# Performance work log

Hardware: AMD Instinct MI355X
Metric: run time of the kernel (lower is better)

The kernel has to match this reference:

```python
import jax, jax.numpy as jnp
import numpy as np

D = 1024
H = 16
DH = D // H
LN_EPS = 1e-5


def setup_inputs() -> dict:
    key = jax.random.key(0)
    ks = jax.random.split(key, 8)
    B, L = 32768, 3
    q = jax.random.normal(ks[0], (B, 1, D), dtype=jnp.float32)
    x = jax.random.normal(ks[1], (B, L, D), dtype=jnp.float32)
    s = 0.02  # weight init scale
    Wq = jax.random.normal(ks[2], (D, D), dtype=jnp.float32) * s
    Wk = jax.random.normal(ks[3], (D, D), dtype=jnp.float32) * s
    Wv = jax.random.normal(ks[4], (D, D), dtype=jnp.float32) * s
    Wr = jax.random.normal(ks[5], (D, D), dtype=jnp.float32) * s
    Wo = jax.random.normal(ks[6], (D, D), dtype=jnp.float32) * s
    ln_gamma = jnp.ones((D,), dtype=jnp.float32)
    ln_beta = jnp.zeros((D,), dtype=jnp.float32)
    return {"q": q, "x": x, "Wq": Wq, "Wk": Wk, "Wv": Wv, "Wr": Wr,
            "Wo": Wo, "ln_gamma": ln_gamma, "ln_beta": ln_beta}


def _layer_norm(y, gamma, beta):
    mu = jnp.mean(y, axis=-1, keepdims=True)
    var = jnp.mean(jnp.square(y - mu), axis=-1, keepdims=True)
    return (y - mu) * jax.lax.rsqrt(var + LN_EPS) * gamma + beta


def reference(q, x, Wq, Wk, Wv, Wr, Wo, ln_gamma, ln_beta):
    # torch Linear(no bias): y = inp @ W^T
    Q = jnp.einsum('bqd,ed->bqe', q, Wq)            # [B,1,D]
    K = jnp.einsum('bld,ed->ble', x, Wk)            # [B,L,D]
    V = jnp.einsum('bld,ed->ble', x, Wv)
    R = jnp.einsum('bld,ed->ble', x, Wr)
    V_eff = jax.nn.sigmoid(R) * V                   # gated V
    B, L = x.shape[0], x.shape[1]
    Qh = Q.reshape(B, 1, H, DH).transpose(0, 2, 1, 3)   # [B,H,1,Dh]
    Kh = K.reshape(B, L, H, DH).transpose(0, 2, 1, 3)   # [B,H,L,Dh]
    Vh = V_eff.reshape(B, L, H, DH).transpose(0, 2, 1, 3)
    scores = jnp.einsum('bhqd,bhld->bhql', Qh, Kh) / jnp.sqrt(jnp.float32(DH))
    attn = jax.nn.softmax(scores, axis=-1)              # [B,H,1,L]; dropout=eval no-op
    out = jnp.einsum('bhql,bhld->bhqd', attn, Vh)       # [B,H,1,Dh]
    out = out.transpose(0, 2, 1, 3).reshape(B, 1, D)
    out = jnp.einsum('bqd,ed->bqe', out, Wo)
    out = _layer_norm(q + out, ln_gamma, ln_beta)
    return out, attn
```

## Files before the change

kernel.cpp:

```cpp
#include <hip/hip_runtime.h>
#include <math.h>


using half8   = __attribute__((ext_vector_type(8))) _Float16;
using half4   = __attribute__((ext_vector_type(4))) _Float16;
using floatx4 = __attribute__((ext_vector_type(4))) float;

#define BTOT 32768
#define DM   1024
#define NH   16
#define LSEQ 3

__device__ __forceinline__ void gload_lds16(const void* g, void* l) {
  __builtin_amdgcn_global_load_lds(
      (const __attribute__((address_space(1))) void*)g,
      (__attribute__((address_space(3))) void*)l, 16, 0, 0);
}

__global__ __launch_bounds__(256) void acvt(
    const float* __restrict__ xc, _Float16* __restrict__ x16,
    const float* __restrict__ qc, _Float16* __restrict__ q16, int xblocks)
{
  const int blk = blockIdx.x;
  const float* src;
  _Float16* dst;
  size_t o;
  if (blk < xblocks) {
    o = ((size_t)blk * 256 + threadIdx.x) * 4;
    src = xc; dst = x16;
  } else {
    o = ((size_t)(blk - xblocks) * 256 + threadIdx.x) * 4;
    src = qc; dst = q16;
  }
  floatx4 a = *(const floatx4*)(src + o);
  half4 h;
  h[0] = (_Float16)a[0]; h[1] = (_Float16)a[1];
  h[2] = (_Float16)a[2]; h[3] = (_Float16)a[3];
  *(half4*)(dst + o) = h;
}

__global__ __launch_bounds__(256) void wconv(
    const float* __restrict__ Wq, const float* __restrict__ Wk,
    const float* __restrict__ Wv, const float* __restrict__ Wr,
    const float* __restrict__ Wo,
    _Float16* __restrict__ Wq16, _Float16* __restrict__ Wkvr16,
    _Float16* __restrict__ Wo16)
{
  const int i = blockIdx.x * 256 + threadIdx.x;
  const size_t o = (size_t)i * 4;
  const size_t M1 = (size_t)1024 * 1024;
  floatx4 a;
  half4 h;
#define CVT(SRC, DST, OFF)                                        \
  a = *(const floatx4*)((SRC) + o);                               \
  h[0] = (_Float16)a[0]; h[1] = (_Float16)a[1];                   \
  h[2] = (_Float16)a[2]; h[3] = (_Float16)a[3];                   \
  *(half4*)((DST) + (OFF) + o) = h;
  CVT(Wq, Wq16, 0)
  CVT(Wo, Wo16, 0)
  CVT(Wk, Wkvr16, 0)
  CVT(Wv, Wkvr16, M1)
  CVT(Wr, Wkvr16, 2 * M1)
#undef CVT
}

template <bool OUT_HALF>
__global__ __launch_bounds__(256) void gemm_bt(
    const _Float16* __restrict__ A, const _Float16* __restrict__ Bw,
    void* __restrict__ Cout, int M, int N, int K)
{
  __shared__ __attribute__((aligned(16))) char As[128 * 128];
  __shared__ __attribute__((aligned(16))) char Bs[128 * 128];

  const int tid  = threadIdx.x;
  const int lane = tid & 63;
  const int wave = tid >> 6;
  const int wr = wave >> 1, wc = wave & 1;
  const int l15 = lane & 15, lk = lane >> 4;

  const int nwg = gridDim.x * gridDim.y;
  int wgid = blockIdx.y * gridDim.x + blockIdx.x;
  wgid = (wgid & 7) * (nwg >> 3) + (wgid >> 3);
  const int bx = wgid % gridDim.x;
  const int by = wgid / gridDim.x;

  const int col0 = bx * 128;
  const int row0 = by * 128;

  floatx4 acc[4][4] = {};

  const int nK = K >> 6;
  for (int kt = 0; kt < nK; ++kt) {
    const int k0 = kt << 6;
    {
      const char* gA = (const char*)A + ((size_t)row0 * K + k0) * 2;
      const char* gB = (const char*)Bw + ((size_t)col0 * K + k0) * 2;
      #pragma unroll
      for (int it = 0; it < 4; ++it) {
        const int off = it * 4096 + tid * 16;
        const int row = off >> 7;
        const int ch  = (off >> 4) & 7;
        const int sch = ch ^ (row & 7);
        gload_lds16(gA + (size_t)row * ((size_t)K * 2) + (sch << 4), As + off);
        gload_lds16(gB + (size_t)row * ((size_t)K * 2) + (sch << 4), Bs + off);
      }
    }
    __syncthreads();
    #pragma unroll
    for (int kk = 0; kk < 64; kk += 32) {
      half8 af[4], bf[4];
      const int c = (kk >> 3) + lk;
      #pragma unroll
      for (int m = 0; m < 4; ++m) {
        const int rw = wr * 64 + m * 16 + l15;
        af[m] = *(const half8*)(As + rw * 128 + ((c ^ (rw & 7)) << 4));
      }
      #pragma unroll
      for (int n = 0; n < 4; ++n) {
        const int rw = wc * 64 + n * 16 + l15;
        bf[n] = *(const half8*)(Bs + rw * 128 + ((c ^ (rw & 7)) << 4));
      }
      #pragma unroll
      for (int m = 0; m < 4; ++m)
        #pragma unroll
        for (int n = 0; n < 4; ++n)
          acc[m][n] = __builtin_amdgcn_mfma_f32_16x16x32_f16(
              af[m], bf[n], acc[m][n], 0, 0, 0);
    }
    __syncthreads();
  }
  #pragma unroll
  for (int m = 0; m < 4; ++m) {
    const int rbase = row0 + wr * 64 + m * 16 + (lk << 2);
    #pragma unroll
    for (int r = 0; r < 4; ++r) {
      const size_t rowoff = (size_t)(rbase + r) * N;
      #pragma unroll
      for (int n = 0; n < 4; ++n) {
        const int col = col0 + wc * 64 + n * 16 + l15;
        const float v = acc[m][n][r];
        if constexpr (OUT_HALF)
          ((_Float16*)Cout)[rowoff + col] = (_Float16)v;
        else
          ((float*)Cout)[rowoff + col] = v;
      }
    }
  }
}

__global__ __launch_bounds__(256) void attn_kernel(
    const _Float16* __restrict__ Q16, const _Float16* __restrict__ KVR,
    _Float16* __restrict__ AV16, float* __restrict__ attn_out,
    size_t batch0)
{
  const int lane = threadIdx.x & 63;
  const int wave = threadIdx.x >> 6;
  const size_t b = (size_t)blockIdx.x * 4 + wave;
  const int h = lane >> 2, p = lane & 3;
  const int doff = h * 64 + p * 16;

  float qv[16];
  {
    const half8* qp = (const half8*)(Q16 + b * 1024 + doff);
    half8 q0 = qp[0], q1 = qp[1];
    #pragma unroll
    for (int i = 0; i < 8; ++i) { qv[i] = (float)q0[i]; qv[8 + i] = (float)q1[i]; }
  }
  float sc[LSEQ];
  #pragma unroll
  for (int l = 0; l < LSEQ; ++l) {
    const half8* kp = (const half8*)(KVR + (b * 3 + l) * 3072 + doff);
    half8 k0 = kp[0], k1 = kp[1];
    float d = 0.f;
    #pragma unroll
    for (int i = 0; i < 8; ++i)
      d += qv[i] * (float)k0[i] + qv[8 + i] * (float)k1[i];
    d += __shfl_xor(d, 1);
    d += __shfl_xor(d, 2);
    sc[l] = d * 0.125f;
  }
  const float mx = fmaxf(sc[0], fmaxf(sc[1], sc[2]));
  const float e0 = __expf(sc[0] - mx), e1 = __expf(sc[1] - mx),
              e2 = __expf(sc[2] - mx);
  const float inv = 1.f / (e0 + e1 + e2);
  const float at0 = e0 * inv, at1 = e1 * inv, at2 = e2 * inv;
  if (p == 0) {
    float* ao = attn_out + ((batch0 + b) * NH + h) * LSEQ;
    ao[0] = at0; ao[1] = at1; ao[2] = at2;
  }
  const float atw[LSEQ] = {at0, at1, at2};
  float av[16] = {};
  #pragma unroll
  for (int l = 0; l < LSEQ; ++l) {
    const half8* vp = (const half8*)(KVR + (b * 3 + l) * 3072 + 1024 + doff);
    const half8* rp = (const half8*)(KVR + (b * 3 + l) * 3072 + 2048 + doff);
    half8 v0 = vp[0], v1 = vp[1], r0 = rp[0], r1 = rp[1];
    #pragma unroll
    for (int i = 0; i < 8; ++i) {
      const float g0 = 1.f / (1.f + __expf(-(float)r0[i]));
      const float g1 = 1.f / (1.f + __expf(-(float)r1[i]));
      av[i]     += atw[l] * g0 * (float)v0[i];
      av[8 + i] += atw[l] * g1 * (float)v1[i];
    }
  }
  half8 o0, o1;
  #pragma unroll
  for (int i = 0; i < 8; ++i) { o0[i] = (_Float16)av[i]; o1[i] = (_Float16)av[8 + i]; }
  half8* op = (half8*)(AV16 + b * 1024 + doff);
  op[0] = o0; op[1] = o1;
}

__global__ __launch_bounds__(256) void ln_kernel(
    const float* __restrict__ qres, const float* __restrict__ outlin,
    const float* __restrict__ gamma, const float* __restrict__ beta,
    float* __restrict__ out)
{
  const int lane = threadIdx.x & 63;
  const size_t r = (size_t)blockIdx.x * 4 + (threadIdx.x >> 6);
  const size_t base = r * 1024 + lane * 16;
  floatx4 y[4];
  float s = 0.f, ss = 0.f;
  #pragma unroll
  for (int i = 0; i < 4; ++i) {
    floatx4 a  = *(const floatx4*)(qres + base + i * 4);
    floatx4 bb = *(const floatx4*)(outlin + base + i * 4);
    y[i] = a + bb;
    #pragma unroll
    for (int j = 0; j < 4; ++j) { s += y[i][j]; ss += y[i][j] * y[i][j]; }
  }
  #pragma unroll
  for (int o = 1; o < 64; o <<= 1) {
    s  += __shfl_xor(s, o);
    ss += __shfl_xor(ss, o);
  }
  const float mu  = s * (1.f / 1024.f);
  const float var = ss * (1.f / 1024.f) - mu * mu;
  const float rs  = rsqrtf(var + 1e-5f);
  #pragma unroll
  for (int i = 0; i < 4; ++i) {
    floatx4 g  = *(const floatx4*)(gamma + lane * 16 + i * 4);
    floatx4 be = *(const floatx4*)(beta + lane * 16 + i * 4);
    floatx4 o;
    #pragma unroll
    for (int j = 0; j < 4; ++j)
      o[j] = (y[i][j] - mu) * rs * g[j] + be[j];
    *(floatx4*)(out + base + i * 4) = o;
  }
}

extern "C" void kernel_launch(void* const* d_in, const int* in_sizes, int n_in,
                              void* d_out, int out_size, void* d_ws, size_t ws_size,
                              hipStream_t stream)
{
  const float* q     = (const float*)d_in[0];
  const float* x     = (const float*)d_in[1];
  const float* Wq    = (const float*)d_in[2];
  const float* Wk    = (const float*)d_in[3];
  const float* Wv    = (const float*)d_in[4];
  const float* Wr    = (const float*)d_in[5];
  const float* Wo    = (const float*)d_in[6];
  const float* gamma = (const float*)d_in[7];
  const float* beta  = (const float*)d_in[8];

  float* out      = (float*)d_out;
  float* attn_out = out + (size_t)BTOT * DM;

  char* ws = (char*)d_ws;
  _Float16* Wq16   = (_Float16*)ws; ws += (size_t)1024 * 1024 * 2;
  _Float16* Wkvr16 = (_Float16*)ws; ws += (size_t)3072 * 1024 * 2;
  _Float16* Wo16   = (_Float16*)ws; ws += (size_t)1024 * 1024 * 2;

  const size_t wbytes = (size_t)10 * 1024 * 1024;
  const size_t rem = ws_size > wbytes ? ws_size - wbytes : 0;
  int CB = 128;
  for (int c = BTOT; c >= 128; c >>= 1)
    if ((size_t)c * 34816 <= rem) { CB = c; break; }

  _Float16* x16  = (_Float16*)ws; ws += (size_t)CB * 3 * 1024 * 2;
  _Float16* q16  = (_Float16*)ws; ws += (size_t)CB * 1024 * 2;
  _Float16* Q16  = (_Float16*)ws; ws += (size_t)CB * 1024 * 2;
  _Float16* KVR  = (_Float16*)ws; ws += (size_t)CB * 3 * 3072 * 2;
  _Float16* AV16 = (_Float16*)ws; ws += (size_t)CB * 1024 * 2;
  float*    OUTL = (float*)ws;

  wconv<<<dim3(1024), dim3(256), 0, stream>>>(Wq, Wk, Wv, Wr, Wo,
                                              Wq16, Wkvr16, Wo16);

  const int xblk = (CB * LSEQ * DM) / 1024;
  const int qblk = (CB * DM) / 1024;
  for (int c = 0; c < BTOT; c += CB) {
    const float* qc = q + (size_t)c * DM;
    const float* xc = x + (size_t)c * LSEQ * DM;
    acvt<<<dim3(xblk + qblk), dim3(256), 0, stream>>>(xc, x16, qc, q16, xblk);
    gemm_bt<true><<<dim3(1024 / 128, CB / 128), dim3(256), 0, stream>>>(
        q16, Wq16, Q16, CB, 1024, 1024);
    gemm_bt<true><<<dim3(3072 / 128, (3 * CB) / 128), dim3(256), 0, stream>>>(
        x16, Wkvr16, KVR, 3 * CB, 3072, 1024);
    attn_kernel<<<dim3(CB / 4), dim3(256), 0, stream>>>(Q16, KVR, AV16,
                                                        attn_out, (size_t)c);
    gemm_bt<false><<<dim3(1024 / 128, CB / 128), dim3(256), 0, stream>>>(
        AV16, Wo16, OUTL, CB, 1024, 1024);
    ln_kernel<<<dim3(CB / 4), dim3(256), 0, stream>>>(qc, OUTL, gamma, beta,
                                                      out + (size_t)c * DM);
  }
}
```

Before: 1.855 ms.

## Add 256x256-tile pipelined GEMM with 8 waves for full-batch path

Adds a new GEMM kernel that uses 256x256 output tiles, 512 threads and 128KB of double-buffered LDS. Loads go straight from global memory into LDS and are interleaved across eight MFMA phases, with explicit vmcnt waits, barriers, priority bumps and a workgroup ID remap. It is used for all three projection GEMMs only when the whole batch fits in the workspace in one chunk. The larger tile raises arithmetic intensity and overlaps copies with compute, at the cost of fewer resident workgroups and hand-scheduled synchronisation that depends on the chunk size.

```diff
diff --git a/kernel.cpp b/kernel.cpp
--- a/kernel.cpp
+++ b/kernel.cpp
@@ -16,6 +16,10 @@
       (const __attribute__((address_space(1))) void*)g,
       (__attribute__((address_space(3))) void*)l, 16, 0, 0);
 }
+
+#define WAITVM(N) do { __builtin_amdgcn_sched_barrier(0);            \
+  asm volatile("s_waitcnt vmcnt(" #N ")" ::: "memory");              \
+  __builtin_amdgcn_sched_barrier(0); } while (0)
 
 __global__ __launch_bounds__(256) void acvt(
     const float* __restrict__ xc, _Float16* __restrict__ x16,
@@ -148,6 +152,138 @@
   }
 }
 
+template <int BUF, int CK, int MH, bool LOADB, typename SF, typename GF>
+__device__ __forceinline__ void phase(const char* ldsp, int aoff, int boff,
+                                      int ca0, int ca1,
+                                      half8 (&bf)[4], floatx4 (&acc)[8][4],
+                                      SF&& stage, GF&& gate)
+{
+  const int ca = CK ? ca1 : ca0;
+  half8 af[4];
+  #pragma unroll
+  for (int m = 0; m < 4; ++m)
+    af[m] = *(const half8*)(ldsp + BUF * 32768 + aoff + (MH * 4 + m) * 2048 + ca);
+  if constexpr (LOADB) {
+    #pragma unroll
+    for (int n = 0; n < 4; ++n)
+      bf[n] = *(const half8*)(ldsp + 65536 + BUF * 32768 + boff + n * 2048 + ca);
+  }
+  stage();
+  gate();
+  __builtin_amdgcn_s_barrier();
+  __builtin_amdgcn_s_setprio(1);
+  #pragma unroll
+  for (int m = 0; m < 4; ++m)
+    #pragma unroll
+    for (int n = 0; n < 4; ++n)
+      acc[MH * 4 + m][n] = __builtin_amdgcn_mfma_f32_16x16x32_f16(
+          af[m], bf[n], acc[MH * 4 + m][n], 0, 0, 0);
+  __builtin_amdgcn_s_setprio(0);
+  __builtin_amdgcn_s_barrier();
+}
+
+template <bool OUT_HALF>
+__global__ __launch_bounds__(512, 2) void gemm256(
+    const _Float16* __restrict__ A, const _Float16* __restrict__ Bw,
+    void* __restrict__ Cout, int M, int N, int K)
+{
+  __shared__ __attribute__((aligned(16))) char lds[131072];
+  const int tid  = threadIdx.x;
+  const int lane = tid & 63;
+  const int wave = tid >> 6;
+  const int wm = wave >> 2, wn = wave & 3;
+  const int l15 = lane & 15, lk = lane >> 4;
+  const int sx = l15 & 7;
+
+  const int nwg = gridDim.x * gridDim.y;
+  int wgid = blockIdx.y * gridDim.x + blockIdx.x;
+  wgid = (wgid & 7) * (nwg >> 3) + (wgid >> 3);
+  const int bx = wgid % gridDim.x;
+  const int by = wgid / gridDim.x;
+  const int col0 = bx * 256, row0 = by * 256;
+
+  const size_t Kb = (size_t)K * 2;
+  const char* gA = (const char*)A + (size_t)row0 * Kb;
+  const char* gB = (const char*)Bw + (size_t)col0 * Kb;
+  char* ldsc = (char*)lds;
+
+  auto stA = [&](int buf, int half, int kt) {
+    #pragma unroll
+    for (int ld = 0; ld < 2; ++ld) {
+      const int off = ld * 8192 + tid * 16;
+      const int r = off >> 7;
+      const int sch = ((off >> 4) & 7) ^ (r & 7);
+      gload_lds16(gA + (size_t)(half * 128 + r) * Kb + kt * 128 + (sch << 4),
+                  ldsc + buf * 32768 + half * 16384 + off);
+    }
+  };
+  auto stB = [&](int buf, int half, int kt) {
+    #pragma unroll
+    for (int ld = 0; ld < 2; ++ld) {
+      const int off = ld * 8192 + tid * 16;
+      const int r = off >> 7;
+      const int sch = ((off >> 4) & 7) ^ (r & 7);
+      gload_lds16(gB + (size_t)(half * 128 + r) * Kb + kt * 128 + (sch << 4),
+                  ldsc + 65536 + buf * 32768 + half * 16384 + off);
+    }
+  };
+
+  const int aoff = (wm * 128 + l15) * 128;
+  const int boff = (wn * 64 + l15) * 128;
+  const int ca0 = (lk ^ sx) << 4;
+  const int ca1 = ((4 + lk) ^ sx) << 4;
+
+  floatx4 acc[8][4] = {};
+  half8 bf[4];
+
+  stA(0, 0, 0); stA(0, 1, 0); stB(0, 0, 0); stB(0, 1, 0);
+  stB(1, 0, 1);
+  WAITVM(2);
+  __builtin_amdgcn_s_barrier();
+
+  const int nIt = K >> 7;
+  for (int it = 0; it < nIt; ++it) {
+    const int t1 = 2 * it + 1, t2 = 2 * it + 2, t3 = 2 * it + 3;
+    const bool lastit = (it == nIt - 1);
+    auto g0 = [&] {};
+    auto g2 = [&] { if (!lastit) { WAITVM(2); } else { WAITVM(0); } };
+    phase<0, 0, 0, true >(ldsc, aoff, boff, ca0, ca1, bf, acc,
+                          [&] { stA(1, 0, t1); }, g0);
+    phase<0, 0, 1, false>(ldsc, aoff, boff, ca0, ca1, bf, acc,
+                          [&] { stA(1, 1, t1); }, g0);
+    phase<0, 1, 0, true >(ldsc, aoff, boff, ca0, ca1, bf, acc,
+                          [&] { stB(1, 1, t1); }, g0);
+    phase<0, 1, 1, false>(ldsc, aoff, boff, ca0, ca1, bf, acc,
+                          [&] { if (!lastit) stB(0, 0, t2); }, g2);
+    phase<1, 0, 0, true >(ldsc, aoff, boff, ca0, ca1, bf, acc,
+                          [&] { if (!lastit) stA(0, 0, t2); }, g0);
+    phase<1, 0, 1, false>(ldsc, aoff, boff, ca0, ca1, bf, acc,
+                          [&] { if (!lastit) stA(0, 1, t2); }, g0);
+    phase<1, 1, 0, true >(ldsc, aoff, boff, ca0, ca1, bf, acc,
+                          [&] { if (!lastit) stB(0, 1, t2); }, g0);
+    phase<1, 1, 1, false>(ldsc, aoff, boff, ca0, ca1, bf, acc,
+                          [&] { if (!lastit) stB(1, 0, t3); }, g2);
+  }
+
+  #pragma unroll
+  for (int m = 0; m < 8; ++m) {
+    const int rbase = row0 + wm * 128 + m * 16 + (lk << 2);
+    #pragma unroll
+    for (int r = 0; r < 4; ++r) {
+      const size_t rowoff = (size_t)(rbase + r) * N;
+      #pragma unroll
+      for (int n = 0; n < 4; ++n) {
+        const int col = col0 + wn * 64 + n * 16 + l15;
+        const float v = acc[m][n][r];
+        if constexpr (OUT_HALF)
+          ((_Float16*)Cout)[rowoff + col] = (_Float16)v;
+        else
+          ((float*)Cout)[rowoff + col] = v;
+      }
+    }
+  }
+}
+
 __global__ __launch_bounds__(256) void attn_kernel(
     const _Float16* __restrict__ Q16, const _Float16* __restrict__ KVR,
     _Float16* __restrict__ AV16, float* __restrict__ attn_out,
@@ -283,6 +419,8 @@
   _Float16* AV16 = (_Float16*)ws; ws += (size_t)CB * 1024 * 2;
   float*    OUTL = (float*)ws;
 
+  const bool big = (CB == BTOT);
+
   wconv<<<dim3(1024), dim3(256), 0, stream>>>(Wq, Wk, Wv, Wr, Wo,
                                               Wq16, Wkvr16, Wo16);
 
@@ -292,14 +430,26 @@
     const float* qc = q + (size_t)c * DM;
     const float* xc = x + (size_t)c * LSEQ * DM;
     acvt<<<dim3(xblk + qblk), dim3(256), 0, stream>>>(xc, x16, qc, q16, xblk);
-    gemm_bt<true><<<dim3(1024 / 128, CB / 128), dim3(256), 0, stream>>>(
-        q16, Wq16, Q16, CB, 1024, 1024);
-    gemm_bt<true><<<dim3(3072 / 128, (3 * CB) / 128), dim3(256), 0, stream>>>(
-        x16, Wkvr16, KVR, 3 * CB, 3072, 1024);
+    if (big) {
+      gemm256<true><<<dim3(1024 / 256, CB / 256), dim3(512), 0, stream>>>(
+          q16, Wq16, Q16, CB, 1024, 1024);
+      gemm256<true><<<dim3(3072 / 256, (3 * CB) / 256), dim3(512), 0, stream>>>(
+          x16, Wkvr16, KVR, 3 * CB, 3072, 1024);
+    } else {
+      gemm_bt<true><<<dim3(1024 / 128, CB / 128), dim3(256), 0, stream>>>(
+          q16, Wq16, Q16, CB, 1024, 1024);
+      gemm_bt<true><<<dim3(3072 / 128, (3 * CB) / 128), dim3(256), 0, stream>>>(
+          x16, Wkvr16, KVR, 3 * CB, 3072, 1024);
+    }
     attn_kernel<<<dim3(CB / 4), dim3(256), 0, stream>>>(Q16, KVR, AV16,
                                                         attn_out, (size_t)c);
-    gemm_bt<false><<<dim3(1024 / 128, CB / 128), dim3(256), 0, stream>>>(
-        AV16, Wo16, OUTL, CB, 1024, 1024);
+    if (big) {
+      gemm256<false><<<dim3(1024 / 256, CB / 256), dim3(512), 0, stream>>>(
+          AV16, Wo16, OUTL, CB, 1024, 1024);
+    } else {
+      gemm_bt<false><<<dim3(1024 / 128, CB / 128), dim3(256), 0, stream>>>(
+          AV16, Wo16, OUTL, CB, 1024, 1024);
+    }
     ln_kernel<<<dim3(CB / 4), dim3(256), 0, stream>>>(qc, OUTL, gamma, beta,
                                                       out + (size_t)c * DM);
   }
```

Result: faster. 1.619 ms (-12.7%).
